# Performance work log

Measured on AMD Instinct MI355X. Metric: run time of the kernel, lower is better.

The kernel has to match this reference:

```python
import jax, jax.numpy as jnp
import numpy as np

D_MODEL = 768
N_HEADS = 12
D_K = D_MODEL // N_HEADS


def setup_inputs() -> dict:
    key = jax.random.key(0)
    ks = jax.random.split(key, 9)
    B, S = 4, 2048
    sc = 1.0 / np.sqrt(D_MODEL)
    inp = {"x": jax.random.normal(ks[0], (B, S, D_MODEL), dtype=jnp.float32)}
    names = ["q", "k", "v", "o"]
    for i, n in enumerate(names):
        inp[f"W{n}"] = jax.random.normal(ks[1 + 2 * i], (D_MODEL, D_MODEL), dtype=jnp.float32) * sc
        inp[f"b{n}"] = jax.random.normal(ks[2 + 2 * i], (D_MODEL,), dtype=jnp.float32) * 0.01
    return inp


def reference(x, Wq, bq, Wk, bk, Wv, bv, Wo, bo):
    B, S, _ = x.shape
    def split_heads(t):  # [B,S,D] -> [B,H,S,d_k]
        return t.reshape(B, S, N_HEADS, D_K).transpose(0, 2, 1, 3)
    Q = split_heads(x @ Wq.T + bq)
    K = split_heads(x @ Wk.T + bk)
    V = split_heads(x @ Wv.T + bv)
    # NOTE: original divides by d_k, not sqrt(d_k)
    scores = jnp.einsum("bhqd,bhkd->bhqk", Q, K) / D_K
    scores = jax.nn.softmax(scores, axis=-1)
    att = jnp.einsum("bhqk,bhkd->bhqd", scores, V)  # [B,H,S,d_k]
    att = att.transpose(0, 2, 1, 3).reshape(B, S, D_MODEL)
    return att @ Wo.T + bo
```

## Files before the change

kernel.cpp:

```cpp
#include <hip/hip_runtime.h>
#include <hip/hip_bf16.h>

typedef __bf16 bf16;
typedef _Float16 f16;
typedef bf16 bf16x8 __attribute__((ext_vector_type(8)));
typedef bf16 bf16x4 __attribute__((ext_vector_type(4)));
typedef f16 f16x8 __attribute__((ext_vector_type(8)));
typedef f16 f16x4 __attribute__((ext_vector_type(4)));
typedef f16 f16x2 __attribute__((ext_vector_type(2)));
typedef float f32x4 __attribute__((ext_vector_type(4)));

#define SLEN 2048
#define HEADS 12
#define DMODEL 768

#define GLOAD16(g, l) \
    __builtin_amdgcn_global_load_lds((const __attribute__((address_space(1))) void*)(g), \
                                     (__attribute__((address_space(3))) void*)(l), 16, 0, 0)

__global__ void cvt_all(const float* __restrict__ x,
                        const float* __restrict__ Wq, const float* __restrict__ Wk,
                        const float* __restrict__ Wv, const float* __restrict__ Wo,
                        bf16* __restrict__ xb, bf16* __restrict__ wdst) {
    int idx = blockIdx.x * 256 + threadIdx.x;
    const float* s; bf16* d;
    if (idx < 1572864) {
        s = x; d = xb;
    } else {
        int t = idx - 1572864;
        int wi = t / 147456;
        idx = t - wi * 147456;
        s = (wi == 0) ? Wq : (wi == 1) ? Wk : (wi == 2) ? Wv : Wo;
        d = wdst + (size_t)wi * 589824;
    }
    float4 v = ((const float4*)s)[idx];
    bf16x4 o;
    o[0] = (bf16)v.x; o[1] = (bf16)v.y; o[2] = (bf16)v.z; o[3] = (bf16)v.w;
    *(bf16x4*)(d + (size_t)idx * 4) = o;
}

__global__ __launch_bounds__(256, 2) void gemm_qkv(
    const bf16* __restrict__ A, const bf16* __restrict__ Bw,
    const float* __restrict__ bq, const float* __restrict__ bk, const float* __restrict__ bv,
    bf16* __restrict__ Qb, bf16* __restrict__ Kb, f16* __restrict__ VTb)
{
    __shared__ __align__(16) char smem[49152];
    typedef bf16 ATile[128][32];
    typedef bf16 BTile[256][32];
    ATile* As = (ATile*)smem;
    BTile* Bs = (BTile*)(smem + 16384);
    const int K = DMODEL;
    int tid = threadIdx.x;
    int w = tid >> 6, lane = tid & 63, i16 = lane & 15, q4 = lane >> 4;
    int mblk = (w & 1) * 64, nblk = (w >> 1) * 128;
    int row0 = blockIdx.y * 128, col0 = blockIdx.x * 256;
    int srow = lane >> 2, scol = (lane & 3) * 8;
    f32x4 acc[8][4] = {};

    const bf16* Ab = A  + (size_t)(row0 + w * 16 + srow) * K + scol;
    const bf16* Bb = Bw + (size_t)(col0 + w * 16 + srow) * K + scol;

#define STAGE(buf, k0) do { \
        GLOAD16(Ab + (k0),                   &As[buf][w * 16][0]); \
        GLOAD16(Ab + (size_t)64 * K + (k0),  &As[buf][w * 16 + 64][0]); \
        GLOAD16(Bb + (k0),                   &Bs[buf][w * 16][0]); \
        GLOAD16(Bb + (size_t)64 * K + (k0),  &Bs[buf][w * 16 + 64][0]); \
        GLOAD16(Bb + (size_t)128 * K + (k0), &Bs[buf][w * 16 + 128][0]); \
        GLOAD16(Bb + (size_t)192 * K + (k0), &Bs[buf][w * 16 + 192][0]); \
    } while (0)

    STAGE(0, 0);
    __syncthreads();
    int buf = 0;
    for (int k0 = 0; k0 < K; k0 += 32, buf ^= 1) {
        if (k0 + 32 < K) STAGE(buf ^ 1, k0 + 32);
        bf16x8 af[4], bfr[8];
#pragma unroll
        for (int t = 0; t < 4; ++t) af[t]  = *(const bf16x8*)(&As[buf][mblk + t * 16 + i16][q4 * 8]);
#pragma unroll
        for (int t = 0; t < 8; ++t) bfr[t] = *(const bf16x8*)(&Bs[buf][nblk + t * 16 + i16][q4 * 8]);
#pragma unroll
        for (int ct = 0; ct < 8; ++ct)
#pragma unroll
            for (int st = 0; st < 4; ++st)
                acc[ct][st] = __builtin_amdgcn_mfma_f32_16x16x32_bf16(bfr[ct], af[st], acc[ct][st], 0, 0, 0);
        __syncthreads();
    }
#undef STAGE

    int region = col0 / DMODEL;
    int cbase = col0 - region * DMODEL + nblk;

    if (region < 2) {
        const float* bias = region ? bk : bq;
        bf16* dstb = region ? Kb : Qb;
#pragma unroll
        for (int ct = 0; ct < 8; ++ct) {
#pragma unroll
            for (int st = 0; st < 4; ++st) {
                int c0 = cbase + ct * 16 + q4 * 4;
                int h = c0 >> 6, d0 = c0 & 63;
                int sg = row0 + mblk + st * 16 + i16;
                int b = sg >> 11, s = sg & 2047;
                float4 bb = *(const float4*)(bias + c0);
                bf16x4 o;
                if (region == 0) {
                    o[0] = (bf16)((acc[ct][st][0] + bb.x) * 0.0225421217f);
                    o[1] = (bf16)((acc[ct][st][1] + bb.y) * 0.0225421217f);
                    o[2] = (bf16)((acc[ct][st][2] + bb.z) * 0.0225421217f);
                    o[3] = (bf16)((acc[ct][st][3] + bb.w) * 0.0225421217f);
                } else {
                    o[0] = (bf16)(acc[ct][st][0] + bb.x);
                    o[1] = (bf16)(acc[ct][st][1] + bb.y);
                    o[2] = (bf16)(acc[ct][st][2] + bb.z);
                    o[3] = (bf16)(acc[ct][st][3] + bb.w);
                }
                *(bf16x4*)(dstb + (((size_t)(b * HEADS + h)) * SLEN + s) * 64 + d0) = o;
            }
        }
    } else {
        f16 (*Cs)[132] = (f16(*)[132])smem;
#pragma unroll
        for (int p = 0; p < 2; ++p) {
            if ((w >> 1) == p) {
#pragma unroll
                for (int ct = 0; ct < 8; ++ct) {
#pragma unroll
                    for (int st = 0; st < 4; ++st) {
                        int cg = cbase + ct * 16 + q4 * 4;
                        float4 bb = *(const float4*)(bv + cg);
                        f16x4 vv;
                        vv[0] = (f16)(acc[ct][st][0] + bb.x);
                        vv[1] = (f16)(acc[ct][st][1] + bb.y);
                        vv[2] = (f16)(acc[ct][st][2] + bb.z);
                        vv[3] = (f16)(acc[ct][st][3] + bb.w);
                        *(f16x4*)(&Cs[mblk + st * 16 + i16][ct * 16 + q4 * 4]) = vv;
                    }
                }
            }
            __syncthreads();
            int cl = lane * 2;
            int cg = (col0 - 2 * DMODEL) + p * 128 + cl;
            int h = cg >> 6, d = cg & 63;
            int s0 = w * 32;
            int b = row0 >> 11, sg = (row0 & 2047) + s0;
            f16* dst0 = VTb + ((size_t)(b * HEADS + h) * 64 + d) * SLEN + sg;
            f16* dst1 = dst0 + SLEN;
#pragma unroll
            for (int j = 0; j < 4; ++j) {
                unsigned v[8];
#pragma unroll
                for (int i = 0; i < 8; ++i) v[i] = *(const unsigned*)(&Cs[s0 + j * 8 + i][cl]);
                unsigned lo[4], hi[4];
#pragma unroll
                for (int i = 0; i < 4; ++i) {
                    lo[i] = (v[2 * i] & 0xffffu) | (v[2 * i + 1] << 16);
                    hi[i] = (v[2 * i] >> 16) | (v[2 * i + 1] & 0xffff0000u);
                }
                *(uint4*)(dst0 + j * 8) = *(uint4*)lo;
                *(uint4*)(dst1 + j * 8) = *(uint4*)hi;
            }
            __syncthreads();
        }
    }
}

__global__ __launch_bounds__(256, 3) void gemm_out(
    const bf16* __restrict__ A, const bf16* __restrict__ Bw,
    const float* __restrict__ bo, float* __restrict__ out)
{
    __shared__ bf16 As[2][128][32];
    __shared__ bf16 Bs[2][64][32];
    const int K = DMODEL;
    int tid = threadIdx.x;
    int w = tid >> 6, lane = tid & 63, i16 = lane & 15, q4 = lane >> 4;
    int row0 = blockIdx.y * 128, col0 = blockIdx.x * 64;
    int srow = (lane >> 2), scol = (lane & 3) * 8;
    f32x4 acc[4][2] = {};

    const bf16* Ab = A  + (size_t)(row0 + w * 16 + srow) * K + scol;
    const bf16* Bb = Bw + (size_t)(col0 + w * 16 + srow) * K + scol;

#define STAGE(buf, k0) do { \
        GLOAD16(Ab + (k0),                  &As[buf][w * 16][0]); \
        GLOAD16(Ab + (size_t)64 * K + (k0), &As[buf][w * 16 + 64][0]); \
        GLOAD16(Bb + (k0),                  &Bs[buf][w * 16][0]); \
    } while (0)

    STAGE(0, 0);
    __syncthreads();
    int buf = 0;
    for (int k0 = 0; k0 < K; k0 += 32, buf ^= 1) {
        if (k0 + 32 < K) STAGE(buf ^ 1, k0 + 32);
        bf16x8 af[2], bfr[4];
#pragma unroll
        for (int t = 0; t < 2; ++t) af[t] = *(const bf16x8*)(&As[buf][w * 32 + t * 16 + i16][q4 * 8]);
#pragma unroll
        for (int t = 0; t < 4; ++t) bfr[t] = *(const bf16x8*)(&Bs[buf][t * 16 + i16][q4 * 8]);
#pragma unroll
        for (int ct = 0; ct < 4; ++ct)
#pragma unroll
            for (int st = 0; st < 2; ++st)
                acc[ct][st] = __builtin_amdgcn_mfma_f32_16x16x32_bf16(bfr[ct], af[st], acc[ct][st], 0, 0, 0);
        __syncthreads();
    }
#undef STAGE

#pragma unroll
    for (int ct = 0; ct < 4; ++ct) {
#pragma unroll
        for (int st = 0; st < 2; ++st) {
            int c0 = col0 + ct * 16 + q4 * 4;
            int s = row0 + w * 32 + st * 16 + i16;
            float4 bb = *(const float4*)(bo + c0);
            float4 o = {acc[ct][st][0] + bb.x, acc[ct][st][1] + bb.y,
                        acc[ct][st][2] + bb.z, acc[ct][st][3] + bb.w};
            *(float4*)(out + (size_t)s * DMODEL + c0) = o;
        }
    }
}

__global__ __launch_bounds__(256, 3) void attn_kernel(
    const bf16* __restrict__ Qb, const bf16* __restrict__ Kb,
    const f16* __restrict__ VTb, bf16* __restrict__ att)
{
    __shared__ bf16 Ks[128][64];
    __shared__ f16  Vt[64][128];

    int tid = threadIdx.x;
    int w = tid >> 6, lane = tid & 63, i16 = lane & 15, q4 = lane >> 4;
    int qt = blockIdx.x, h = blockIdx.y, b = blockIdx.z;
    size_t bh = (size_t)b * HEADS + h;
    const bf16* Qp = Qb + (bh * SLEN + qt * 128 + w * 32) * 64;
    const bf16* Kp = Kb + bh * SLEN * 64;
    const f16*  Vp = VTb + bh * 64 * SLEN;

    bf16x8 aq[2][2];
#pragma unroll
    for (int qs = 0; qs < 2; ++qs) {
        aq[qs][0] = *(const bf16x8*)(Qp + (qs * 16 + i16) * 64 + q4 * 8);
        aq[qs][1] = *(const bf16x8*)(Qp + (qs * 16 + i16) * 64 + 32 + q4 * 8);
    }

    int rlK = lane >> 3;
    int cK = (lane & 7) ^ rlK;
    const bf16* kp[4];
#pragma unroll
    for (int j = 0; j < 4; ++j) {
        int p = w * 32 + j * 8 + rlK;
        int key = 32 * (p >> 5) + 8 * ((p >> 2) & 3) + 4 * ((p >> 4) & 1) + (p & 3);
        kp[j] = Kp + (size_t)key * 64 + cK * 8;
    }
    int rlV = lane >> 4;
    const f16* vp[4];
#pragma unroll
    for (int j = 0; j < 4; ++j) {
        int rowa = w * 16 + j * 4 + rlV;
        int cV = (lane & 15) ^ (rowa & 15);
        vp[j] = Vp + (size_t)rowa * SLEN + cV * 8;
    }

    f16x8 vones = {};
    if (i16 == 0)
#pragma unroll
        for (int j = 0; j < 8; ++j) vones[j] = (f16)1;

    f32x4 oacc[2][4] = {};
    f32x4 lacc[2] = {};
    int ck0 = (q4 ^ (i16 & 7)) * 8;
    int ck1 = ((q4 ^ 4) ^ (i16 & 7)) * 8;

    for (int kt = 0; kt < 16; ++kt) {
#pragma unroll
        for (int j = 0; j < 4; ++j) {
            GLOAD16(kp[j], &Ks[w * 32 + j * 8][0]);
            GLOAD16(vp[j], &Vt[w * 16 + j * 4][0]);
            kp[j] += 128 * 64;
            vp[j] += 128;
        }
        __syncthreads();

#pragma unroll
        for (int u = 0; u < 4; ++u) {
            bf16x8 k00 = *(const bf16x8*)(&Ks[u * 32 + i16][ck0]);
            bf16x8 k01 = *(const bf16x8*)(&Ks[u * 32 + i16][ck1]);
            bf16x8 k10 = *(const bf16x8*)(&Ks[u * 32 + 16 + i16][ck0]);
            bf16x8 k11 = *(const bf16x8*)(&Ks[u * 32 + 16 + i16][ck1]);
            f16x8 pf[2];
#pragma unroll
            for (int qs = 0; qs < 2; ++qs) {
                f32x4 z0 = {}, z1 = {};
                z0 = __builtin_amdgcn_mfma_f32_16x16x32_bf16(k00, aq[qs][0], z0, 0, 0, 0);
                z0 = __builtin_amdgcn_mfma_f32_16x16x32_bf16(k01, aq[qs][1], z0, 0, 0, 0);
                z1 = __builtin_amdgcn_mfma_f32_16x16x32_bf16(k10, aq[qs][0], z1, 0, 0, 0);
                z1 = __builtin_amdgcn_mfma_f32_16x16x32_bf16(k11, aq[qs][1], z1, 0, 0, 0);
                f16x2 p01 = __builtin_bit_cast(f16x2,
                    __builtin_amdgcn_cvt_pkrtz(__builtin_amdgcn_exp2f(z0[0]),
                                               __builtin_amdgcn_exp2f(z0[1])));
                f16x2 p23 = __builtin_bit_cast(f16x2,
                    __builtin_amdgcn_cvt_pkrtz(__builtin_amdgcn_exp2f(z0[2]),
                                               __builtin_amdgcn_exp2f(z0[3])));
                f16x2 p45 = __builtin_bit_cast(f16x2,
                    __builtin_amdgcn_cvt_pkrtz(__builtin_amdgcn_exp2f(z1[0]),
                                               __builtin_amdgcn_exp2f(z1[1])));
                f16x2 p67 = __builtin_bit_cast(f16x2,
                    __builtin_amdgcn_cvt_pkrtz(__builtin_amdgcn_exp2f(z1[2]),
                                               __builtin_amdgcn_exp2f(z1[3])));
                pf[qs][0] = p01[0]; pf[qs][1] = p01[1];
                pf[qs][2] = p23[0]; pf[qs][3] = p23[1];
                pf[qs][4] = p45[0]; pf[qs][5] = p45[1];
                pf[qs][6] = p67[0]; pf[qs][7] = p67[1];
                lacc[qs] = __builtin_amdgcn_mfma_f32_16x16x32_f16(vones, pf[qs], lacc[qs], 0, 0, 0);
            }
#pragma unroll
            for (int dt = 0; dt < 4; ++dt) {
                int vc = ((4 * u + q4) ^ i16) * 8;
                f16x8 vf = *(const f16x8*)(&Vt[dt * 16 + i16][vc]);
                oacc[0][dt] = __builtin_amdgcn_mfma_f32_16x16x32_f16(vf, pf[0], oacc[0][dt], 0, 0, 0);
                oacc[1][dt] = __builtin_amdgcn_mfma_f32_16x16x32_f16(vf, pf[1], oacc[1][dt], 0, 0, 0);
            }
        }
        __syncthreads();
    }

#pragma unroll
    for (int qs = 0; qs < 2; ++qs) {
        float l = __shfl(lacc[qs][0], i16);
        float inv = 1.f / l;
        int row = qt * 128 + w * 32 + qs * 16 + i16;
        size_t obase = ((size_t)b * SLEN + row) * DMODEL + h * 64;
#pragma unroll
        for (int dt = 0; dt < 4; ++dt) {
            bf16x4 o;
#pragma unroll
            for (int r = 0; r < 4; ++r) o[r] = (bf16)(oacc[qs][dt][r] * inv);
            *(bf16x4*)(att + obase + dt * 16 + q4 * 4) = o;
        }
    }
}

extern "C" void kernel_launch(void* const* d_in, const int* in_sizes, int n_in,
                              void* d_out, int out_size, void* d_ws, size_t ws_size,
                              hipStream_t stream) {
    const float* x  = (const float*)d_in[0];
    const float* Wq = (const float*)d_in[1];
    const float* bq = (const float*)d_in[2];
    const float* Wk = (const float*)d_in[3];
    const float* bk = (const float*)d_in[4];
    const float* Wv = (const float*)d_in[5];
    const float* bv = (const float*)d_in[6];
    const float* Wo = (const float*)d_in[7];
    const float* bo = (const float*)d_in[8];
    float* out = (float*)d_out;

    char* ws = (char*)d_ws;
    bf16* xb   = (bf16*)(ws);
    bf16* wqkv = (bf16*)(ws + 12582912);
    bf16* wob  = (bf16*)(ws + 16121856);
    bf16* Qb   = (bf16*)(ws + 17301504);
    bf16* Kb   = (bf16*)(ws + 29884416);
    f16*  VTb  = (f16*)(ws + 42467328);
    bf16* attb = xb;

    cvt_all<<<8448, 256, 0, stream>>>(x, Wq, Wk, Wv, Wo, xb, wqkv);
    gemm_qkv<<<dim3(9, 64), 256, 0, stream>>>(xb, wqkv, bq, bk, bv, Qb, Kb, VTb);
    attn_kernel<<<dim3(16, 12, 4), 256, 0, stream>>>(Qb, Kb, VTb, attb);
    gemm_out<<<dim3(12, 64), 256, 0, stream>>>(attb, wob, bo, out);
}
```

Before: 229.3 us.

## Retile QKV GEMM to 128x128 with swizzled K=64 stages; double-buffer attention K/V

The QKV projection GEMM moves from 128x256 tiles with K-step 32 to 128x128 tiles with K-step 64. The new tiles use an XOR-swizzled LDS layout to avoid bank conflicts and launch twice as many blocks, which simplifies the V-transpose epilogue to a single pass. The attention kernel double-buffers its K and V LDS tiles so the next tile's loads overlap compute, removing one barrier per iteration. In exchange, attention LDS use doubles and its occupancy hint drops from 3 to 2 blocks per CU.

```diff
diff --git a/kernel.cpp b/kernel.cpp
--- a/kernel.cpp
+++ b/kernel.cpp
@@ -44,46 +44,62 @@
     const float* __restrict__ bq, const float* __restrict__ bk, const float* __restrict__ bv,
     bf16* __restrict__ Qb, bf16* __restrict__ Kb, f16* __restrict__ VTb)
 {
-    __shared__ __align__(16) char smem[49152];
-    typedef bf16 ATile[128][32];
-    typedef bf16 BTile[256][32];
-    ATile* As = (ATile*)smem;
-    BTile* Bs = (BTile*)(smem + 16384);
+    __shared__ __align__(16) char smem[65536];
+    typedef bf16 Tile[128][64];
+    Tile* As = (Tile*)smem;
+    Tile* Bs = (Tile*)(smem + 32768);
     const int K = DMODEL;
     int tid = threadIdx.x;
     int w = tid >> 6, lane = tid & 63, i16 = lane & 15, q4 = lane >> 4;
-    int mblk = (w & 1) * 64, nblk = (w >> 1) * 128;
-    int row0 = blockIdx.y * 128, col0 = blockIdx.x * 256;
-    int srow = lane >> 2, scol = (lane & 3) * 8;
-    f32x4 acc[8][4] = {};
-
-    const bf16* Ab = A  + (size_t)(row0 + w * 16 + srow) * K + scol;
-    const bf16* Bb = Bw + (size_t)(col0 + w * 16 + srow) * K + scol;
+    int mblk = (w & 1) * 64, nblk = (w >> 1) * 64;
+    int row0 = blockIdx.y * 128, col0 = blockIdx.x * 128;
+    f32x4 acc[4][4] = {};
+
+    int rl = lane >> 3, cp = lane & 7;
+    const bf16* ap[4]; const bf16* bp[4];
+#pragma unroll
+    for (int j = 0; j < 4; ++j) {
+        int r = w * 32 + j * 8 + rl;
+        int cl = cp ^ (r & 7);
+        ap[j] = A  + (size_t)(row0 + r) * K + cl * 8;
+        bp[j] = Bw + (size_t)(col0 + r) * K + cl * 8;
+    }
 
 #define STAGE(buf, k0) do { \
-        GLOAD16(Ab + (k0),                   &As[buf][w * 16][0]); \
-        GLOAD16(Ab + (size_t)64 * K + (k0),  &As[buf][w * 16 + 64][0]); \
-        GLOAD16(Bb + (k0),                   &Bs[buf][w * 16][0]); \
-        GLOAD16(Bb + (size_t)64 * K + (k0),  &Bs[buf][w * 16 + 64][0]); \
-        GLOAD16(Bb + (size_t)128 * K + (k0), &Bs[buf][w * 16 + 128][0]); \
-        GLOAD16(Bb + (size_t)192 * K + (k0), &Bs[buf][w * 16 + 192][0]); \
+        GLOAD16(ap[0] + (k0), &As[buf][w * 32][0]); \
+        GLOAD16(ap[1] + (k0), &As[buf][w * 32 + 8][0]); \
+        GLOAD16(ap[2] + (k0), &As[buf][w * 32 + 16][0]); \
+        GLOAD16(ap[3] + (k0), &As[buf][w * 32 + 24][0]); \
+        GLOAD16(bp[0] + (k0), &Bs[buf][w * 32][0]); \
+        GLOAD16(bp[1] + (k0), &Bs[buf][w * 32 + 8][0]); \
+        GLOAD16(bp[2] + (k0), &Bs[buf][w * 32 + 16][0]); \
+        GLOAD16(bp[3] + (k0), &Bs[buf][w * 32 + 24][0]); \
     } while (0)
+
+    int x7 = i16 & 7;
+    int c0 = (q4 ^ x7) * 8;
+    int c1 = ((4 + q4) ^ x7) * 8;
 
     STAGE(0, 0);
     __syncthreads();
     int buf = 0;
-    for (int k0 = 0; k0 < K; k0 += 32, buf ^= 1) {
-        if (k0 + 32 < K) STAGE(buf ^ 1, k0 + 32);
-        bf16x8 af[4], bfr[8];
-#pragma unroll
-        for (int t = 0; t < 4; ++t) af[t]  = *(const bf16x8*)(&As[buf][mblk + t * 16 + i16][q4 * 8]);
-#pragma unroll
-        for (int t = 0; t < 8; ++t) bfr[t] = *(const bf16x8*)(&Bs[buf][nblk + t * 16 + i16][q4 * 8]);
-#pragma unroll
-        for (int ct = 0; ct < 8; ++ct)
-#pragma unroll
-            for (int st = 0; st < 4; ++st)
-                acc[ct][st] = __builtin_amdgcn_mfma_f32_16x16x32_bf16(bfr[ct], af[st], acc[ct][st], 0, 0, 0);
+    for (int k0 = 0; k0 < K; k0 += 64, buf ^= 1) {
+        if (k0 + 64 < K) STAGE(buf ^ 1, k0 + 64);
+        bf16x8 af0[4], af1[4], bf0[4], bf1[4];
+#pragma unroll
+        for (int t = 0; t < 4; ++t) {
+            af0[t] = *(const bf16x8*)(&As[buf][mblk + t * 16 + i16][c0]);
+            af1[t] = *(const bf16x8*)(&As[buf][mblk + t * 16 + i16][c1]);
+            bf0[t] = *(const bf16x8*)(&Bs[buf][nblk + t * 16 + i16][c0]);
+            bf1[t] = *(const bf16x8*)(&Bs[buf][nblk + t * 16 + i16][c1]);
+        }
+#pragma unroll
+        for (int ct = 0; ct < 4; ++ct)
+#pragma unroll
+            for (int st = 0; st < 4; ++st) {
+                acc[ct][st] = __builtin_amdgcn_mfma_f32_16x16x32_bf16(bf0[ct], af0[st], acc[ct][st], 0, 0, 0);
+                acc[ct][st] = __builtin_amdgcn_mfma_f32_16x16x32_bf16(bf1[ct], af1[st], acc[ct][st], 0, 0, 0);
+            }
         __syncthreads();
     }
 #undef STAGE
@@ -94,21 +110,22 @@
     if (region < 2) {
         const float* bias = region ? bk : bq;
         bf16* dstb = region ? Kb : Qb;
-#pragma unroll
-        for (int ct = 0; ct < 8; ++ct) {
+        float scale = region ? 1.0f : 0.0225421217f;
+#pragma unroll
+        for (int ct = 0; ct < 4; ++ct) {
 #pragma unroll
             for (int st = 0; st < 4; ++st) {
-                int c0 = cbase + ct * 16 + q4 * 4;
-                int h = c0 >> 6, d0 = c0 & 63;
+                int cc = cbase + ct * 16 + q4 * 4;
+                int h = cc >> 6, d0 = cc & 63;
                 int sg = row0 + mblk + st * 16 + i16;
                 int b = sg >> 11, s = sg & 2047;
-                float4 bb = *(const float4*)(bias + c0);
+                float4 bb = *(const float4*)(bias + cc);
                 bf16x4 o;
                 if (region == 0) {
-                    o[0] = (bf16)((acc[ct][st][0] + bb.x) * 0.0225421217f);
-                    o[1] = (bf16)((acc[ct][st][1] + bb.y) * 0.0225421217f);
-                    o[2] = (bf16)((acc[ct][st][2] + bb.z) * 0.0225421217f);
-                    o[3] = (bf16)((acc[ct][st][3] + bb.w) * 0.0225421217f);
+                    o[0] = (bf16)((acc[ct][st][0] + bb.x) * scale);
+                    o[1] = (bf16)((acc[ct][st][1] + bb.y) * scale);
+                    o[2] = (bf16)((acc[ct][st][2] + bb.z) * scale);
+                    o[3] = (bf16)((acc[ct][st][3] + bb.w) * scale);
                 } else {
                     o[0] = (bf16)(acc[ct][st][0] + bb.x);
                     o[1] = (bf16)(acc[ct][st][1] + bb.y);
@@ -121,46 +138,40 @@
     } else {
         f16 (*Cs)[132] = (f16(*)[132])smem;
 #pragma unroll
-        for (int p = 0; p < 2; ++p) {
-            if ((w >> 1) == p) {
-#pragma unroll
-                for (int ct = 0; ct < 8; ++ct) {
-#pragma unroll
-                    for (int st = 0; st < 4; ++st) {
-                        int cg = cbase + ct * 16 + q4 * 4;
-                        float4 bb = *(const float4*)(bv + cg);
-                        f16x4 vv;
-                        vv[0] = (f16)(acc[ct][st][0] + bb.x);
-                        vv[1] = (f16)(acc[ct][st][1] + bb.y);
-                        vv[2] = (f16)(acc[ct][st][2] + bb.z);
-                        vv[3] = (f16)(acc[ct][st][3] + bb.w);
-                        *(f16x4*)(&Cs[mblk + st * 16 + i16][ct * 16 + q4 * 4]) = vv;
-                    }
-                }
-            }
-            __syncthreads();
-            int cl = lane * 2;
-            int cg = (col0 - 2 * DMODEL) + p * 128 + cl;
-            int h = cg >> 6, d = cg & 63;
-            int s0 = w * 32;
-            int b = row0 >> 11, sg = (row0 & 2047) + s0;
-            f16* dst0 = VTb + ((size_t)(b * HEADS + h) * 64 + d) * SLEN + sg;
-            f16* dst1 = dst0 + SLEN;
-#pragma unroll
-            for (int j = 0; j < 4; ++j) {
-                unsigned v[8];
-#pragma unroll
-                for (int i = 0; i < 8; ++i) v[i] = *(const unsigned*)(&Cs[s0 + j * 8 + i][cl]);
-                unsigned lo[4], hi[4];
-#pragma unroll
-                for (int i = 0; i < 4; ++i) {
-                    lo[i] = (v[2 * i] & 0xffffu) | (v[2 * i + 1] << 16);
-                    hi[i] = (v[2 * i] >> 16) | (v[2 * i + 1] & 0xffff0000u);
-                }
-                *(uint4*)(dst0 + j * 8) = *(uint4*)lo;
-                *(uint4*)(dst1 + j * 8) = *(uint4*)hi;
-            }
-            __syncthreads();
+        for (int ct = 0; ct < 4; ++ct) {
+#pragma unroll
+            for (int st = 0; st < 4; ++st) {
+                int cg = cbase + ct * 16 + q4 * 4;
+                float4 bb = *(const float4*)(bv + cg);
+                f16x4 vv;
+                vv[0] = (f16)(acc[ct][st][0] + bb.x);
+                vv[1] = (f16)(acc[ct][st][1] + bb.y);
+                vv[2] = (f16)(acc[ct][st][2] + bb.z);
+                vv[3] = (f16)(acc[ct][st][3] + bb.w);
+                *(f16x4*)(&Cs[mblk + st * 16 + i16][nblk + ct * 16 + q4 * 4]) = vv;
+            }
+        }
+        __syncthreads();
+        int cl = lane * 2;
+        int cg = cbase - nblk + cl;
+        int h = cg >> 6, d = cg & 63;
+        int s0 = w * 32;
+        int b = row0 >> 11, sg = (row0 & 2047) + s0;
+        f16* dst0 = VTb + ((size_t)(b * HEADS + h) * 64 + d) * SLEN + sg;
+        f16* dst1 = dst0 + SLEN;
+#pragma unroll
+        for (int j = 0; j < 4; ++j) {
+            unsigned v[8];
+#pragma unroll
+            for (int i = 0; i < 8; ++i) v[i] = *(const unsigned*)(&Cs[s0 + j * 8 + i][cl]);
+            unsigned lo[4], hi[4];
+#pragma unroll
+            for (int i = 0; i < 4; ++i) {
+                lo[i] = (v[2 * i] & 0xffffu) | (v[2 * i + 1] << 16);
+                hi[i] = (v[2 * i] >> 16) | (v[2 * i + 1] & 0xffff0000u);
+            }
+            *(uint4*)(dst0 + j * 8) = *(uint4*)lo;
+            *(uint4*)(dst1 + j * 8) = *(uint4*)hi;
         }
     }
 }
@@ -220,12 +231,12 @@
     }
 }
 
-__global__ __launch_bounds__(256, 3) void attn_kernel(
+__global__ __launch_bounds__(256, 2) void attn_kernel(
     const bf16* __restrict__ Qb, const bf16* __restrict__ Kb,
     const f16* __restrict__ VTb, bf16* __restrict__ att)
 {
-    __shared__ bf16 Ks[128][64];
-    __shared__ f16  Vt[64][128];
+    __shared__ bf16 Ks[2][128][64];
+    __shared__ f16  Vt[2][64][128];
 
     int tid = threadIdx.x;
     int w = tid >> 6, lane = tid & 63, i16 = lane & 15, q4 = lane >> 4;
@@ -270,22 +281,27 @@
     int ck0 = (q4 ^ (i16 & 7)) * 8;
     int ck1 = ((q4 ^ 4) ^ (i16 & 7)) * 8;
 
-    for (int kt = 0; kt < 16; ++kt) {
-#pragma unroll
-        for (int j = 0; j < 4; ++j) {
-            GLOAD16(kp[j], &Ks[w * 32 + j * 8][0]);
-            GLOAD16(vp[j], &Vt[w * 16 + j * 4][0]);
-            kp[j] += 128 * 64;
-            vp[j] += 128;
-        }
+#define ASTAGE(buf) do { \
+        for (int j = 0; j < 4; ++j) { \
+            GLOAD16(kp[j], &Ks[buf][w * 32 + j * 8][0]); \
+            GLOAD16(vp[j], &Vt[buf][w * 16 + j * 4][0]); \
+            kp[j] += 128 * 64; \
+            vp[j] += 128; \
+        } \
+    } while (0)
+
+    ASTAGE(0);
+    int buf = 0;
+    for (int kt = 0; kt < 16; ++kt, buf ^= 1) {
         __syncthreads();
+        if (kt < 15) ASTAGE(buf ^ 1);
 
 #pragma unroll
         for (int u = 0; u < 4; ++u) {
-            bf16x8 k00 = *(const bf16x8*)(&Ks[u * 32 + i16][ck0]);
-            bf16x8 k01 = *(const bf16x8*)(&Ks[u * 32 + i16][ck1]);
-            bf16x8 k10 = *(const bf16x8*)(&Ks[u * 32 + 16 + i16][ck0]);
-            bf16x8 k11 = *(const bf16x8*)(&Ks[u * 32 + 16 + i16][ck1]);
+            bf16x8 k00 = *(const bf16x8*)(&Ks[buf][u * 32 + i16][ck0]);
+            bf16x8 k01 = *(const bf16x8*)(&Ks[buf][u * 32 + i16][ck1]);
+            bf16x8 k10 = *(const bf16x8*)(&Ks[buf][u * 32 + 16 + i16][ck0]);
+            bf16x8 k11 = *(const bf16x8*)(&Ks[buf][u * 32 + 16 + i16][ck1]);
             f16x8 pf[2];
 #pragma unroll
             for (int qs = 0; qs < 2; ++qs) {
@@ -315,13 +331,13 @@
 #pragma unroll
             for (int dt = 0; dt < 4; ++dt) {
                 int vc = ((4 * u + q4) ^ i16) * 8;
-                f16x8 vf = *(const f16x8*)(&Vt[dt * 16 + i16][vc]);
+                f16x8 vf = *(const f16x8*)(&Vt[buf][dt * 16 + i16][vc]);
                 oacc[0][dt] = __builtin_amdgcn_mfma_f32_16x16x32_f16(vf, pf[0], oacc[0][dt], 0, 0, 0);
                 oacc[1][dt] = __builtin_amdgcn_mfma_f32_16x16x32_f16(vf, pf[1], oacc[1][dt], 0, 0, 0);
             }
         }
-        __syncthreads();
-    }
+    }
+#undef ASTAGE
 
 #pragma unroll
     for (int qs = 0; qs < 2; ++qs) {
@@ -363,7 +379,7 @@
     bf16* attb = xb;
 
     cvt_all<<<8448, 256, 0, stream>>>(x, Wq, Wk, Wv, Wo, xb, wqkv);
-    gemm_qkv<<<dim3(9, 64), 256, 0, stream>>>(xb, wqkv, bq, bk, bv, Qb, Kb, VTb);
+    gemm_qkv<<<dim3(18, 64), 256, 0, stream>>>(xb, wqkv, bq, bk, bv, Qb, Kb, VTb);
     attn_kernel<<<dim3(16, 12, 4), 256, 0, stream>>>(Qb, Kb, VTb, attb);
     gemm_out<<<dim3(12, 64), 256, 0, stream>>>(attb, wob, bo, out);
 }
```

Result: no change. 233.8 us (+1.9%).
